# Kernel optimization log

Measured on AMD Instinct MI355X. Metric: run time of the kernel, lower is better.

Reference implementation:

```python
import jax, jax.numpy as jnp
import numpy as np

NEAR, FAR = 0.1, 10.0
R, S = 65536, 192

def setup_inputs() -> dict:
    key = jax.random.key(0)
    k1, k2, k3, k4 = jax.random.split(key, 4)
    densities = jax.random.normal(k1, (R, S), dtype=jnp.float32)
    colors = jax.random.uniform(k2, (R, S, 3), dtype=jnp.float32)
    # t_vals must be sorted increasing along sample axis (dists = diff)
    t_vals = jnp.sort(NEAR + (FAR - NEAR) * jax.random.uniform(k3, (R, S), dtype=jnp.float32), axis=-1)
    ray_directions = jax.random.normal(k4, (R, 3), dtype=jnp.float32)
    return {"densities": densities, "colors": colors, "t_vals": t_vals,
            "ray_directions": ray_directions}

def reference(densities, colors, t_vals, ray_directions):
    # distances between consecutive samples; last dist = 1e10 (to infinity)
    dists = t_vals[..., 1:] - t_vals[..., :-1]                       # [R, S-1]
    dists = jnp.concatenate([dists, jnp.full_like(dists[..., :1], 1e10)], axis=-1)  # [R, S]
    dists = dists * jnp.linalg.norm(ray_directions, axis=-1, keepdims=True)
    alpha = 1.0 - jnp.exp(-jax.nn.relu(densities) * dists)           # [R, S]
    # exclusive cumulative transmittance: T_i = prod_{j<i} (1 - alpha_j)
    trans = jnp.cumprod(1.0 - alpha + 1e-10, axis=-1)                # [R, S]
    trans = jnp.concatenate([jnp.ones_like(trans[..., :1]), trans[..., :-1]], axis=-1)
    weights = alpha * trans                                          # [R, S]
    rgb = jnp.sum(weights[..., None] * colors, axis=-2)              # [R, 3]
    depth = jnp.sum(weights * t_vals, axis=-1)                       # [R]
    acc_weights = jnp.sum(weights, axis=-1)                          # [R]
    return (rgb, depth, weights, alpha, acc_weights)
```

## Files before the change

### kernel.cpp

```cpp
#include <hip/hip_runtime.h>


#define NUM_S 192

__global__ __launch_bounds__(256) void volrend_kernel(
    const float* __restrict__ dens,
    const float* __restrict__ cols,
    const float* __restrict__ tv,
    const float* __restrict__ rdir,
    float* __restrict__ out_rgb,
    float* __restrict__ out_depth,
    float* __restrict__ out_w,
    float* __restrict__ out_alpha,
    float* __restrict__ out_acc,
    int R)
{
    const int wid  = (blockIdx.x * blockDim.x + threadIdx.x) >> 6;
    const int lane = threadIdx.x & 63;
    if (wid >= R) return;
    const int r = wid;

    const float dx = rdir[r * 3 + 0];
    const float dy = rdir[r * 3 + 1];
    const float dz = rdir[r * 3 + 2];
    const float nrm = sqrtf(dx * dx + dy * dy + dz * dz);

    float carry = 1.0f;
    float acc_r = 0.0f, acc_g = 0.0f, acc_b = 0.0f;
    float acc_d = 0.0f, acc_w = 0.0f;

    const long base = (long)r * NUM_S;

    #pragma unroll
    for (int c = 0; c < 3; ++c) {
        const int s = c * 64 + lane;
        const float t = tv[base + s];

        float tn = __shfl_down(t, 1);
        float dist;
        if (s == NUM_S - 1) {
            dist = 1e10f;
        } else if (lane == 63) {
            dist = tv[base + s + 1] - t;
        } else {
            dist = tn - t;
        }
        dist *= nrm;

        const float d = dens[base + s];
        const float a = 1.0f - __expf(-fmaxf(d, 0.0f) * dist);
        float f = 1.0f - a + 1e-10f;

        float p = f;
        #pragma unroll
        for (int off = 1; off < 64; off <<= 1) {
            float q = __shfl_up(p, off);
            if (lane >= off) p *= q;
        }
        float excl = __shfl_up(p, 1);
        float trans = carry * ((lane == 0) ? 1.0f : excl);

        const float w = a * trans;
        out_w[base + s]     = w;
        out_alpha[base + s] = a;

        const long cb = (base + s) * 3;
        acc_r += w * cols[cb + 0];
        acc_g += w * cols[cb + 1];
        acc_b += w * cols[cb + 2];
        acc_d += w * t;
        acc_w += w;

        carry *= __shfl(p, 63);
    }

    #pragma unroll
    for (int off = 32; off > 0; off >>= 1) {
        acc_r += __shfl_down(acc_r, off);
        acc_g += __shfl_down(acc_g, off);
        acc_b += __shfl_down(acc_b, off);
        acc_d += __shfl_down(acc_d, off);
        acc_w += __shfl_down(acc_w, off);
    }
    if (lane == 0) {
        out_rgb[r * 3 + 0] = acc_r;
        out_rgb[r * 3 + 1] = acc_g;
        out_rgb[r * 3 + 2] = acc_b;
        out_depth[r] = acc_d;
        out_acc[r]   = acc_w;
    }
}

extern "C" void kernel_launch(void* const* d_in, const int* in_sizes, int n_in,
                              void* d_out, int out_size, void* d_ws, size_t ws_size,
                              hipStream_t stream) {
    const float* dens = (const float*)d_in[0];
    const float* cols = (const float*)d_in[1];
    const float* tv   = (const float*)d_in[2];
    const float* rdir = (const float*)d_in[3];

    const int R = in_sizes[3] / 3;
    float* out       = (float*)d_out;
    float* out_rgb   = out;
    float* out_depth = out_rgb + (long)R * 3;
    float* out_w     = out_depth + R;
    float* out_alpha = out_w + (long)R * NUM_S;
    float* out_acc   = out_alpha + (long)R * NUM_S;

    const int threads = 256;
    const int rays_per_block = threads / 64;
    const int blocks = (R + rays_per_block - 1) / rays_per_block;
    volrend_kernel<<<blocks, threads, 0, stream>>>(
        dens, cols, tv, rdir, out_rgb, out_depth, out_w, out_alpha, out_acc, R);
}
```

Baseline: 69.59 us.

## Assign contiguous triples of samples per lane and run a single warp scan

Each lane now owns three consecutive samples instead of striding by 64, so densities, t-values and colors are read as contiguous 12- and 36-byte chunks per lane. The transmittance product is computed serially within each lane and then a single 64-lane inclusive scan runs, replacing three scans and the carry shuffles. This cuts shuffle and latency overhead, but per-lane float3 accesses are not naturally aligned vector loads, so coalescing may be less clean than the strided layout.

After: 68.71 us. About the same (-1.3%).

```diff
diff --git a/kernel.cpp b/kernel.cpp
--- a/kernel.cpp
+++ b/kernel.cpp
@@ -2,6 +2,8 @@
 
 
 #define NUM_S 192
+
+struct f3 { float x, y, z; };
 
 __global__ __launch_bounds__(256) void volrend_kernel(
     const float* __restrict__ dens,
@@ -18,76 +20,71 @@
     const int wid  = (blockIdx.x * blockDim.x + threadIdx.x) >> 6;
     const int lane = threadIdx.x & 63;
     if (wid >= R) return;
-    const int r = wid;
 
-    const float dx = rdir[r * 3 + 0];
-    const float dy = rdir[r * 3 + 1];
-    const float dz = rdir[r * 3 + 2];
-    const float nrm = sqrtf(dx * dx + dy * dy + dz * dz);
+    const long base = (long)wid * NUM_S;
+    const int  s0   = 3 * lane;
 
-    float carry = 1.0f;
-    float acc_r = 0.0f, acc_g = 0.0f, acc_b = 0.0f;
-    float acc_d = 0.0f, acc_w = 0.0f;
+    const f3 t  = *(const f3*)(tv   + base + s0);
+    const f3 d  = *(const f3*)(dens + base + s0);
+    const float* cp = cols + (base + s0) * 3;
+    const f3 c0 = *(const f3*)(cp + 0);
+    const f3 c1 = *(const f3*)(cp + 3);
+    const f3 c2 = *(const f3*)(cp + 6);
+    const f3 rd = *(const f3*)(rdir + (long)wid * 3);
 
-    const long base = (long)r * NUM_S;
+    const float nrm = sqrtf(rd.x * rd.x + rd.y * rd.y + rd.z * rd.z);
 
+    const float tnext = __shfl_down(t.x, 1);
+    const float dist0 = (t.y - t.x) * nrm;
+    const float dist1 = (t.z - t.y) * nrm;
+    const float dist2 = (lane == 63) ? 1e10f * nrm : (tnext - t.z) * nrm;
+
+    const float a0 = 1.0f - __expf(-fmaxf(d.x, 0.0f) * dist0);
+    const float a1 = 1.0f - __expf(-fmaxf(d.y, 0.0f) * dist1);
+    const float a2 = 1.0f - __expf(-fmaxf(d.z, 0.0f) * dist2);
+
+    const float f0 = 1.0f - a0 + 1e-10f;
+    const float f1 = 1.0f - a1 + 1e-10f;
+    const float f2 = 1.0f - a2 + 1e-10f;
+    const float f01 = f0 * f1;
+
+    float P = f01 * f2;
     #pragma unroll
-    for (int c = 0; c < 3; ++c) {
-        const int s = c * 64 + lane;
-        const float t = tv[base + s];
+    for (int off = 1; off < 64; off <<= 1) {
+        const float q = __shfl_up(P, off);
+        if (lane >= off) P *= q;
+    }
+    float excl = __shfl_up(P, 1);
+    if (lane == 0) excl = 1.0f;
 
-        float tn = __shfl_down(t, 1);
-        float dist;
-        if (s == NUM_S - 1) {
-            dist = 1e10f;
-        } else if (lane == 63) {
-            dist = tv[base + s + 1] - t;
-        } else {
-            dist = tn - t;
-        }
-        dist *= nrm;
+    const float w0 = a0 * excl;
+    const float w1 = a1 * excl * f0;
+    const float w2 = a2 * excl * f01;
 
-        const float d = dens[base + s];
-        const float a = 1.0f - __expf(-fmaxf(d, 0.0f) * dist);
-        float f = 1.0f - a + 1e-10f;
+    f3 wv; wv.x = w0; wv.y = w1; wv.z = w2;
+    f3 av; av.x = a0; av.y = a1; av.z = a2;
+    *(f3*)(out_w     + base + s0) = wv;
+    *(f3*)(out_alpha + base + s0) = av;
 
-        float p = f;
-        #pragma unroll
-        for (int off = 1; off < 64; off <<= 1) {
-            float q = __shfl_up(p, off);
-            if (lane >= off) p *= q;
-        }
-        float excl = __shfl_up(p, 1);
-        float trans = carry * ((lane == 0) ? 1.0f : excl);
-
-        const float w = a * trans;
-        out_w[base + s]     = w;
-        out_alpha[base + s] = a;
-
-        const long cb = (base + s) * 3;
-        acc_r += w * cols[cb + 0];
-        acc_g += w * cols[cb + 1];
-        acc_b += w * cols[cb + 2];
-        acc_d += w * t;
-        acc_w += w;
-
-        carry *= __shfl(p, 63);
-    }
+    float acc_r = w0 * c0.x + w1 * c1.x + w2 * c2.x;
+    float acc_g = w0 * c0.y + w1 * c1.y + w2 * c2.y;
+    float acc_b = w0 * c0.z + w1 * c1.z + w2 * c2.z;
+    float acc_d = w0 * t.x + w1 * t.y + w2 * t.z;
+    float acc_w = w0 + w1 + w2;
 
     #pragma unroll
     for (int off = 32; off > 0; off >>= 1) {
-        acc_r += __shfl_down(acc_r, off);
-        acc_g += __shfl_down(acc_g, off);
-        acc_b += __shfl_down(acc_b, off);
-        acc_d += __shfl_down(acc_d, off);
-        acc_w += __shfl_down(acc_w, off);
+        acc_r += __shfl_xor(acc_r, off);
+        acc_g += __shfl_xor(acc_g, off);
+        acc_b += __shfl_xor(acc_b, off);
+        acc_d += __shfl_xor(acc_d, off);
+        acc_w += __shfl_xor(acc_w, off);
     }
     if (lane == 0) {
-        out_rgb[r * 3 + 0] = acc_r;
-        out_rgb[r * 3 + 1] = acc_g;
-        out_rgb[r * 3 + 2] = acc_b;
-        out_depth[r] = acc_d;
-        out_acc[r]   = acc_w;
+        f3 rgb; rgb.x = acc_r; rgb.y = acc_g; rgb.z = acc_b;
+        *(f3*)(out_rgb + (long)wid * 3) = rgb;
+        out_depth[wid] = acc_d;
+        out_acc[wid]   = acc_w;
     }
 }
 
```
